# Optimization experiments

Hardware: AMD Instinct MI355X
Metric: run time of the kernel (lower is better)

## Reference

```python
import jax, jax.numpy as jnp
import numpy as np

B, S, H = 2, 2048, 1024
NQ, NKV, HD = 16, 4, 64
I, E, TOP_K = 3584, 8, 2
SLIDING_WINDOW = 512
EPS = 1e-5
MAX_WAVELENGTH = 10000.0


def setup_inputs() -> dict:
    key = jax.random.key(0)
    ks = jax.random.split(key, 10)
    p = lambda k, shape: jax.random.normal(k, shape, jnp.float32) * 0.02
    return {
        "decoder_sequence": jax.random.normal(ks[0], (B, S, H), jnp.float32),
        "norm1_scale": jnp.ones((H,), jnp.float32),
        "norm2_scale": jnp.ones((H,), jnp.float32),
        "wq": p(ks[1], (H, NQ, HD)),
        "wk": p(ks[2], (H, NKV, HD)),
        "wv": p(ks[3], (H, NKV, HD)),
        "wo": p(ks[4], (NQ, HD, H)),
        "w_router": p(ks[5], (H, E)),
        "w_gate": p(ks[6], (E, H, I)),
        "w_up": p(ks[7], (E, H, I)),
        "w_down": p(ks[8], (E, I, H)),
    }


def _rms_norm(x, scale, eps=EPS):
    x32 = x.astype(jnp.float32)
    var = jnp.mean(x32 * x32, axis=-1, keepdims=True)
    return (x32 * jax.lax.rsqrt(var + eps) * scale).astype(x.dtype)


def _rope(x):
    # x: [B, S, n_heads, head_dim]; keras-hub RotaryEmbedding (interleaved cos/sin,
    # half-split rotate then interleave via stack+reshape).
    seq_len, dim = x.shape[1], x.shape[3]
    inv_freq = 1.0 / (MAX_WAVELENGTH ** (jnp.arange(0, dim, 2, dtype=jnp.float32) / dim))
    freq = jnp.arange(seq_len, dtype=jnp.float32)[:, None] * inv_freq[None, :]  # [S, D/2]
    emb = jnp.stack((freq, freq), axis=-1).reshape(seq_len, dim)  # interleaved [S, D]
    cos = jnp.cos(emb)[None, :, None, :].astype(x.dtype)
    sin = jnp.sin(emb)[None, :, None, :].astype(x.dtype)
    x1, x2 = jnp.split(x, 2, axis=-1)
    half_rot = jnp.stack((-x2, x1), axis=-1).reshape(x.shape)
    return x * cos + half_rot * sin


def _forward(x, norm1_scale, norm2_scale, wq, wk, wv, wo, w_router, w_gate, w_up, w_down):
    b, s, h = x.shape
    # --- self attention block ---
    resid = x
    hs = _rms_norm(x, norm1_scale)
    q = jnp.einsum("bsh,hnd->bsnd", hs, wq)
    k = jnp.einsum("bsh,hnd->bsnd", hs, wk)
    v = jnp.einsum("bsh,hnd->bsnd", hs, wv)
    q, k = _rope(q), _rope(k)
    rep = q.shape[2] // k.shape[2]  # GQA group size
    k = jnp.repeat(k, rep, axis=2)
    v = jnp.repeat(v, rep, axis=2)
    scores = jnp.einsum("bqnd,bknd->bnqk", q, k) / jnp.sqrt(jnp.asarray(q.shape[-1], q.dtype))
    qi = jnp.arange(s)[:, None]
    ki = jnp.arange(s)[None, :]
    mask = (ki <= qi) & (ki > qi - SLIDING_WINDOW)  # causal + sliding window
    scores = jnp.where(mask[None, None], scores, jnp.asarray(-1e9, scores.dtype))
    probs = jax.nn.softmax(scores, axis=-1)
    attn = jnp.einsum("bnqk,bknd->bqnd", probs, v)
    x = jnp.einsum("bqnd,ndh->bqh", attn, wo) + resid
    # --- sparse MoE block ---
    resid = x
    hs = _rms_norm(x, norm2_scale)
    h2 = hs.reshape(-1, h)  # [T, H]
    router_logits = h2 @ w_router  # [T, E]
    rw = jax.nn.softmax(router_logits, axis=-1)
    topw, topi = jax.lax.top_k(rw, TOP_K)
    topw = topw / jnp.sum(topw, axis=-1, keepdims=True)
    t = h2.shape[0]
    combine = jnp.zeros((t, E), h2.dtype).at[jnp.arange(t)[:, None], topi].set(topw)
    out = jnp.zeros_like(h2)
    for e in range(E):  # fixed small expert loop; zero combine weight == not routed
        g = jax.nn.silu(h2 @ w_gate[e])
        u = h2 @ w_up[e]
        out = out + combine[:, e:e + 1] * ((u * g) @ w_down[e])
    decoder_output = out.reshape(b, s, h) + resid
    return decoder_output, router_logits


def reference(decoder_sequence, norm1_scale, norm2_scale, wq, wk, wv, wo,
              w_router, w_gate, w_up, w_down):
    return _forward(decoder_sequence, norm1_scale, norm2_scale, wq, wk, wv, wo,
                    w_router, w_gate, w_up, w_down)
```

## Files before the change

kernel.cpp:

```cpp
#include <hip/hip_runtime.h>
#include <hip/hip_bf16.h>
#include <cstdio>


typedef __bf16 bf16x8 __attribute__((ext_vector_type(8)));
typedef float f32x4 __attribute__((ext_vector_type(4)));

#define MFMA16(a, b, c) __builtin_amdgcn_mfma_f32_16x16x32_bf16((a), (b), (c), 0, 0, 0)
#define GL16(g, l)                                                             \
  __builtin_amdgcn_global_load_lds(                                            \
      (const __attribute__((address_space(1))) void*)(g),                      \
      (__attribute__((address_space(3))) void*)(l), 16, 0, 0)
#define WAIT_VM0() asm volatile("s_waitcnt vmcnt(0)" ::: "memory")
#define SETPRIO(n) __builtin_amdgcn_s_setprio(n)
#define PIPE_SYNC(n)                                                           \
  do {                                                                         \
    asm volatile("s_waitcnt vmcnt(" #n ")" ::: "memory");                      \
    __builtin_amdgcn_s_barrier();                                              \
    asm volatile("" ::: "memory");                                             \
  } while (0)

__device__ __forceinline__ unsigned short f2bf(float f) {
  unsigned u = __builtin_bit_cast(unsigned, f);
  u += 0x7fffu + ((u >> 16) & 1u);
  return (unsigned short)(u >> 16);
}
__device__ __forceinline__ float bf2f(unsigned short h) {
  unsigned u = ((unsigned)h) << 16;
  return __builtin_bit_cast(float, u);
}
__device__ __forceinline__ int sw32(int row, int chunk) {
  return row * 32 + ((chunk ^ ((row >> 1) & 3)) * 8);
}

static constexpr size_t O_WQKVT_HI = 0;
static constexpr size_t SZ_WQKVT   = 1536UL * 1024 * 2;
static constexpr size_t O_WQKVT_LO = O_WQKVT_HI + SZ_WQKVT;
static constexpr size_t O_WOT_HI   = O_WQKVT_LO + SZ_WQKVT;
static constexpr size_t SZ_WOT     = 1024UL * 1024 * 2;
static constexpr size_t O_WOT_LO   = O_WOT_HI + SZ_WOT;
static constexpr size_t O_WGT      = O_WOT_LO + SZ_WOT;
static constexpr size_t SZ_WE      = 8UL * 3584 * 1024 * 2;
static constexpr size_t O_WUT      = O_WGT + SZ_WE;
static constexpr size_t O_WDT      = O_WUT + SZ_WE;
static constexpr size_t O_H2       = O_WDT + SZ_WE;
static constexpr size_t SZ_BF_TH   = 4096UL * 1024 * 2;
static constexpr size_t O_TOK      = O_H2 + SZ_BF_TH;
static constexpr size_t O_WGTL     = O_TOK + 8UL * 4096 * 4;
static constexpr size_t O_CNT      = O_WGTL + 8UL * 4096 * 4;
static constexpr size_t O_DYN      = O_CNT + 256;
static constexpr size_t O_HSHI  = O_DYN;
static constexpr size_t O_HSLO  = O_HSHI + SZ_BF_TH;
static constexpr size_t O_QKV   = O_HSLO + SZ_BF_TH;
static constexpr size_t O_QHI   = O_QKV + 4096UL * 1536 * 4;
static constexpr size_t O_QLO   = O_QHI + SZ_BF_TH;
static constexpr size_t O_KHI   = O_QLO + SZ_BF_TH;
static constexpr size_t SZ_BF_T256 = 4096UL * 256 * 2;
static constexpr size_t O_KLO   = O_KHI + SZ_BF_T256;
static constexpr size_t O_VTH   = O_KLO + SZ_BF_T256;
static constexpr size_t O_VTL   = O_VTH + SZ_BF_T256;
static constexpr size_t O_AHI   = O_VTL + SZ_BF_T256;
static constexpr size_t O_ALO   = O_AHI + SZ_BF_TH;
static constexpr size_t O_XATTN = O_ALO + SZ_BF_TH;
static constexpr size_t O_END   = O_XATTN + 4096UL * 1024 * 4;
static constexpr size_t O_ACT   = O_DYN;
static constexpr size_t WS_NEED = O_END;

__global__ void zero_cnt_kernel(int* c) {
  if (threadIdx.x < 8) c[threadIdx.x] = 0;
}

__global__ __launch_bounds__(256) void init_out_kernel(const float* __restrict__ x,
                                                       float* __restrict__ o) {
  const long i = (long)blockIdx.x * 256 + threadIdx.x;
  *(float4*)&o[i * 4] = *(const float4*)&x[i * 4];
}

__global__ __launch_bounds__(256) void rmsnorm_kernel(const float* __restrict__ x,
                                                      const float* __restrict__ scale,
                                                      unsigned short* __restrict__ hi,
                                                      unsigned short* __restrict__ lo) {
  const int t = blockIdx.x, tid = threadIdx.x;
  const float4 v = *(const float4*)&x[(long)t * 1024 + tid * 4];
  float ss = v.x * v.x + v.y * v.y + v.z * v.z + v.w * v.w;
#pragma unroll
  for (int off = 32; off >= 1; off >>= 1) ss += __shfl_down(ss, off);
  __shared__ float red[4];
  if ((tid & 63) == 0) red[tid >> 6] = ss;
  __syncthreads();
  const float r = rsqrtf((red[0] + red[1] + red[2] + red[3]) * (1.0f / 1024.0f) + 1e-5f);
  const float4 sc = *(const float4*)&scale[tid * 4];
  float o[4] = {v.x * r * sc.x, v.y * r * sc.y, v.z * r * sc.z, v.w * r * sc.w};
  ushort4 hh, ll;
  unsigned short* hp = (unsigned short*)&hh;
  unsigned short* lp = (unsigned short*)&ll;
#pragma unroll
  for (int i = 0; i < 4; ++i) {
    hp[i] = f2bf(o[i]);
    lp[i] = f2bf(o[i] - bf2f(hp[i]));
  }
  *(ushort4*)&hi[(long)t * 1024 + tid * 4] = hh;
  if (lo) *(ushort4*)&lo[(long)t * 1024 + tid * 4] = ll;
}

__global__ __launch_bounds__(256) void transpose_cvt(const float* __restrict__ src,
                                                     unsigned short* __restrict__ dst,
                                                     int R, int C, long zsrc, long zdst) {
  src += (long)blockIdx.z * zsrc;
  dst += (long)blockIdx.z * zdst;
  const int c0 = blockIdx.x * 64, r0 = blockIdx.y * 64, tid = threadIdx.x;
  __shared__ float tb[64][65];
#pragma unroll
  for (int p = 0; p < 4; ++p) {
    const int r = p * 16 + (tid >> 4), c = (tid & 15) * 4;
    const float4 v = *(const float4*)&src[(long)(r0 + r) * C + c0 + c];
    tb[c + 0][r] = v.x; tb[c + 1][r] = v.y; tb[c + 2][r] = v.z; tb[c + 3][r] = v.w;
  }
  __syncthreads();
  const int dr = tid >> 2, s0 = (tid & 3) * 16;
  __align__(16) unsigned short tmp[16];
#pragma unroll
  for (int i = 0; i < 16; ++i) tmp[i] = f2bf(tb[dr][s0 + i]);
  const long o = (long)(c0 + dr) * R + r0 + s0;
  *(uint4*)&dst[o] = *(const uint4*)&tmp[0];
  *(uint4*)&dst[o + 8] = *(const uint4*)&tmp[8];
}

__global__ __launch_bounds__(256) void transpose_cvt_split(const float* __restrict__ src,
                                                           unsigned short* __restrict__ dh,
                                                           unsigned short* __restrict__ dl,
                                                           int R, int C) {
  const int c0 = blockIdx.x * 64, r0 = blockIdx.y * 64, tid = threadIdx.x;
  __shared__ float tb[64][65];
#pragma unroll
  for (int p = 0; p < 4; ++p) {
    const int r = p * 16 + (tid >> 4), c = (tid & 15) * 4;
    const float4 v = *(const float4*)&src[(long)(r0 + r) * C + c0 + c];
    tb[c + 0][r] = v.x; tb[c + 1][r] = v.y; tb[c + 2][r] = v.z; tb[c + 3][r] = v.w;
  }
  __syncthreads();
  const int dr = tid >> 2, s0 = (tid & 3) * 16;
  __align__(16) unsigned short th[16], tl[16];
#pragma unroll
  for (int i = 0; i < 16; ++i) {
    const float f = tb[dr][s0 + i];
    th[i] = f2bf(f);
    tl[i] = f2bf(f - bf2f(th[i]));
  }
  const long o = (long)(c0 + dr) * R + r0 + s0;
  *(uint4*)&dh[o] = *(const uint4*)&th[0];
  *(uint4*)&dh[o + 8] = *(const uint4*)&th[8];
  *(uint4*)&dl[o] = *(const uint4*)&tl[0];
  *(uint4*)&dl[o + 8] = *(const uint4*)&tl[8];
}

__global__ __launch_bounds__(256) void gemm_split(const unsigned short* __restrict__ Ahi,
                                                  const unsigned short* __restrict__ Alo,
                                                  const unsigned short* __restrict__ Bhi,
                                                  const unsigned short* __restrict__ Blo,
                                                  const float* __restrict__ resid,
                                                  float* __restrict__ C,
                                                  int M, int N, int K) {
  __shared__ unsigned short Ash[2][4096], Asl[2][4096], Bsh[2][4096], Bsl[2][4096];
  const int tid = threadIdx.x, wid = tid >> 6, lane = tid & 63;
  const int m0 = blockIdx.y * 128, n0 = blockIdx.x * 128;
  const int wm = (wid >> 1) * 64, wn = (wid & 1) * 64;
  const int fr = lane & 15, fg = lane >> 4;
  const int srow = tid >> 2;
  const int scol = (((tid & 3) ^ ((tid >> 3) & 3))) * 8;
  const long aoff = (long)(m0 + srow) * K + scol;
  const long boff = (long)(n0 + srow) * K + scol;
  const long h64 = 64L * K;
  char* a0 = (char*)Ash[0] + wid * 1024; char* a1 = (char*)Ash[1] + wid * 1024;
  char* al0 = (char*)Asl[0] + wid * 1024; char* al1 = (char*)Asl[1] + wid * 1024;
  char* b0 = (char*)Bsh[0] + wid * 1024; char* b1 = (char*)Bsh[1] + wid * 1024;
  char* bl0 = (char*)Bsl[0] + wid * 1024; char* bl1 = (char*)Bsl[1] + wid * 1024;
#define GS_STAGE(koff, pah_, pal_, pbh_, pbl_)                                 \
  do {                                                                         \
    GL16(Ahi + aoff + (koff), (pah_));                                         \
    GL16(Ahi + aoff + h64 + (koff), (pah_) + 4096);                            \
    GL16(Alo + aoff + (koff), (pal_));                                         \
    GL16(Alo + aoff + h64 + (koff), (pal_) + 4096);                            \
    GL16(Bhi + boff + (koff), (pbh_));                                         \
    GL16(Bhi + boff + h64 + (koff), (pbh_) + 4096);                            \
    GL16(Blo + boff + (koff), (pbl_));                                         \
    GL16(Blo + boff + h64 + (koff), (pbl_) + 4096);                            \
  } while (0)
  f32x4 acc[4][4] = {};
  GS_STAGE(0, a0, al0, b0, bl0);
  WAIT_VM0();
  __syncthreads();
  int cur = 0;
  for (int k0 = 0; k0 < K; k0 += 32) {
    const int kn = k0 + 32;
    if (kn < K) {
      if (cur) GS_STAGE(kn, a0, al0, b0, bl0);
      else     GS_STAGE(kn, a1, al1, b1, bl1);
    }
    const unsigned short* As_ = Ash[cur];
    const unsigned short* Al_ = Asl[cur];
    const unsigned short* Bs_ = Bsh[cur];
    const unsigned short* Bl_ = Bsl[cur];
    bf16x8 ah[4], al[4], bh[4], bl[4];
#pragma unroll
    for (int i = 0; i < 4; ++i) {
      const int oA = sw32(wm + i * 16 + fr, fg);
      const int oB = sw32(wn + i * 16 + fr, fg);
      ah[i] = *(const bf16x8*)&As_[oA];
      al[i] = *(const bf16x8*)&Al_[oA];
      bh[i] = *(const bf16x8*)&Bs_[oB];
      bl[i] = *(const bf16x8*)&Bl_[oB];
    }
    SETPRIO(1);
#pragma unroll
    for (int i = 0; i < 4; ++i)
#pragma unroll
      for (int j = 0; j < 4; ++j) {
        acc[i][j] = MFMA16(al[i], bh[j], acc[i][j]);
        acc[i][j] = MFMA16(ah[i], bl[j], acc[i][j]);
        acc[i][j] = MFMA16(ah[i], bh[j], acc[i][j]);
      }
    SETPRIO(0);
    WAIT_VM0();
    __syncthreads();
    cur ^= 1;
  }
#undef GS_STAGE
  const int cr = fg * 4;
#pragma unroll
  for (int i = 0; i < 4; ++i)
#pragma unroll
    for (int j = 0; j < 4; ++j)
#pragma unroll
      for (int rr = 0; rr < 4; ++rr) {
        const int row = m0 + wm + i * 16 + cr + rr;
        const int col = n0 + wn + j * 16 + fr;
        float v = acc[i][j][rr];
        if (resid) v += resid[(long)row * N + col];
        C[(long)row * N + col] = v;
      }
}

__global__ __launch_bounds__(256) void rope_kernel(const float* __restrict__ qkv,
                                                   unsigned short* __restrict__ Qh,
                                                   unsigned short* __restrict__ Ql,
                                                   unsigned short* __restrict__ Kh,
                                                   unsigned short* __restrict__ Kl) {
  const int t = blockIdx.x, b = t >> 11, s = t & 2047;
  const float* src = qkv + (long)t * 1536;
  for (int task = threadIdx.x; task < 640; task += 256) {
    const int head = task >> 5, p = task & 31;
    const float* hp = src + head * 64;
    const float inv = (float)exp2(-(double)p * 0.4152410118609203);
    const float f = (float)s * inv;
    float sn, cs;
    sincosf(f, &sn, &cs);
    const float x0 = hp[2 * p], x1 = hp[2 * p + 1], xa = hp[p], xb = hp[32 + p];
    float o0 = x0 * cs - xb * sn;
    float o1 = x1 * cs + xa * sn;
    unsigned short *dh, *dl;
    long base;
    if (head < 16) {
      o0 *= 0.125f; o1 *= 0.125f;
      base = ((long)(b * 16 + head) * 2048 + s) * 64;
      dh = Qh; dl = Ql;
    } else {
      base = ((long)(b * 4 + (head - 16)) * 2048 + s) * 64;
      dh = Kh; dl = Kl;
    }
    unsigned short h0 = f2bf(o0);
    dh[base + 2 * p] = h0; dl[base + 2 * p] = f2bf(o0 - bf2f(h0));
    unsigned short h1 = f2bf(o1);
    dh[base + 2 * p + 1] = h1; dl[base + 2 * p + 1] = f2bf(o1 - bf2f(h1));
  }
}

__global__ __launch_bounds__(256) void vt_split_kernel(const float* __restrict__ qkv,
                                                       unsigned short* __restrict__ Vh,
                                                       unsigned short* __restrict__ Vl) {
  const int st = blockIdx.x * 64, g = blockIdx.y, b = blockIdx.z, tid = threadIdx.x;
  __shared__ float tb[64][65];
  const float* src = qkv + (long)(b * 2048 + st) * 1536 + 1280 + g * 64;
#pragma unroll
  for (int p = 0; p < 4; ++p) {
    const int r = p * 16 + (tid >> 4), c = (tid & 15) * 4;
    const float4 v = *(const float4*)&src[(long)r * 1536 + c];
    tb[c + 0][r] = v.x; tb[c + 1][r] = v.y; tb[c + 2][r] = v.z; tb[c + 3][r] = v.w;
  }
  __syncthreads();
  const int dr = tid >> 2, s0 = (tid & 3) * 16;
  __align__(16) unsigned short hh[16], ll[16];
#pragma unroll
  for (int i = 0; i < 16; ++i) {
    const float f = tb[dr][s0 + i];
    hh[i] = f2bf(f);
    ll[i] = f2bf(f - bf2f(hh[i]));
  }
  const long dst = ((long)(b * 4 + g) * 64 + dr) * 2048 + st + s0;
  *(uint4*)&Vh[dst] = *(const uint4*)&hh[0];
  *(uint4*)&Vh[dst + 8] = *(const uint4*)&hh[8];
  *(uint4*)&Vl[dst] = *(const uint4*)&ll[0];
  *(uint4*)&Vl[dst + 8] = *(const uint4*)&ll[8];
}

__global__ __launch_bounds__(256) void attn_kernel(const unsigned short* __restrict__ Qh,
                                                   const unsigned short* __restrict__ Ql,
                                                   const unsigned short* __restrict__ Kh,
                                                   const unsigned short* __restrict__ Kl,
                                                   const unsigned short* __restrict__ Vh,
                                                   const unsigned short* __restrict__ Vl,
                                                   unsigned short* __restrict__ Ohi,
                                                   unsigned short* __restrict__ Olo) {
  const int qt = blockIdx.x, h = blockIdx.y, b = blockIdx.z, g = h >> 2;
  const int q0 = qt * 64, tid = threadIdx.x, wid = tid >> 6, lane = tid & 63;
  const int fr = lane & 15, fg = lane >> 4;
  __shared__ unsigned short Ksh[2][2048], Ksl[2][2048];
  __shared__ unsigned short Vsh[2][2048], Vsl[2][2048];
  __shared__ unsigned short Ph[4][512], Pl[4][512];

  const long qoff = ((long)(b * 16 + h) * 2048 + q0 + wid * 16 + fr) * 64;
  bf16x8 qh[2], ql[2];
  qh[0] = *(const bf16x8*)&Qh[qoff + fg * 8];
  qh[1] = *(const bf16x8*)&Qh[qoff + 32 + fg * 8];
  ql[0] = *(const bf16x8*)&Ql[qoff + fg * 8];
  ql[1] = *(const bf16x8*)&Ql[qoff + 32 + fg * 8];

  f32x4 o[4] = {};
  float mrow[4], lrow[4];
#pragma unroll
  for (int rr = 0; rr < 4; ++rr) { mrow[rr] = -1e30f; lrow[rr] = 0.f; }

  const int jmin = (q0 >= 511) ? (q0 - 511) : 0;
  const int jt0 = jmin & ~31;
  const long kbase = ((long)(b * 4 + g) * 2048) * 64;
  const long vbase = ((long)(b * 4 + g) * 64) * 2048;
  const int srK = tid >> 3;
  const int scK = (((tid & 7) ^ (srK & 7))) * 8;
  const int srV = tid >> 2;
  const int scV = (((tid & 3) ^ ((srV >> 1) & 3))) * 8;
  char* kh0 = (char*)Ksh[0] + wid * 1024; char* kh1 = (char*)Ksh[1] + wid * 1024;
  char* kl0 = (char*)Ksl[0] + wid * 1024; char* kl1 = (char*)Ksl[1] + wid * 1024;
  char* vh0 = (char*)Vsh[0] + wid * 1024; char* vh1 = (char*)Vsh[1] + wid * 1024;
  char* vl0 = (char*)Vsl[0] + wid * 1024; char* vl1 = (char*)Vsl[1] + wid * 1024;
#define ATTN_STAGE(jt_, kh_, kl_, vh_, vl_)                                    \
  do {                                                                         \
    const long ko = kbase + (long)((jt_) + srK) * 64 + scK;                    \
    GL16(Kh + ko, (kh_));                                                      \
    GL16(Kl + ko, (kl_));                                                      \
    const long vo = vbase + (long)srV * 2048 + (jt_) + scV;                    \
    GL16(Vh + vo, (vh_));                                                      \
    GL16(Vl + vo, (vl_));                                                      \
  } while (0)

  ATTN_STAGE(jt0, kh0, kl0, vh0, vl0);
  WAIT_VM0();
  __syncthreads();
  int cur = 0;
  for (int jt = jt0; jt < q0 + 64; jt += 32) {
    const int jn = jt + 32;
    if (jn < q0 + 64) {
      if (cur) ATTN_STAGE(jn, kh0, kl0, vh0, vl0);
      else     ATTN_STAGE(jn, kh1, kl1, vh1, vl1);
    }
    const unsigned short* KH = Ksh[cur];
    const unsigned short* KL = Ksl[cur];
    const unsigned short* VH = Vsh[cur];
    const unsigned short* VL = Vsl[cur];

    f32x4 sf[2] = {};
#pragma unroll
    for (int cf = 0; cf < 2; ++cf)
#pragma unroll
      for (int dc = 0; dc < 2; ++dc) {
        const int row = cf * 16 + fr;
        const int off = row * 64 + (((dc * 4 + fg) ^ (row & 7)) * 8);
        const bf16x8 kh = *(const bf16x8*)&KH[off];
        const bf16x8 kl = *(const bf16x8*)&KL[off];
        sf[cf] = MFMA16(ql[dc], kh, sf[cf]);
        sf[cf] = MFMA16(qh[dc], kl, sf[cf]);
        sf[cf] = MFMA16(qh[dc], kh, sf[cf]);
      }

    float sv[2][4];
#pragma unroll
    for (int cf = 0; cf < 2; ++cf) {
      const int j = jt + cf * 16 + fr;
#pragma unroll
      for (int rr = 0; rr < 4; ++rr) {
        const int q = q0 + wid * 16 + fg * 4 + rr;
        const bool ok = (j <= q) && (j >= q - 511);
        sv[cf][rr] = ok ? sf[cf][rr] : -1e30f;
      }
    }
    float scl_[4];
#pragma unroll
    for (int rr = 0; rr < 4; ++rr) {
      float mx = fmaxf(sv[0][rr], sv[1][rr]);
      mx = fmaxf(mx, __shfl_xor(mx, 1));
      mx = fmaxf(mx, __shfl_xor(mx, 2));
      mx = fmaxf(mx, __shfl_xor(mx, 4));
      mx = fmaxf(mx, __shfl_xor(mx, 8));
      const float mn = fmaxf(mrow[rr], mx);
      scl_[rr] = __expf(mrow[rr] - mn);
      mrow[rr] = mn;
    }
    float ps[2][4], rs[4] = {0.f, 0.f, 0.f, 0.f};
#pragma unroll
    for (int cf = 0; cf < 2; ++cf)
#pragma unroll
      for (int rr = 0; rr < 4; ++rr) {
        const float p = (sv[cf][rr] > -1e29f) ? __expf(sv[cf][rr] - mrow[rr]) : 0.f;
        ps[cf][rr] = p;
        rs[rr] += p;
      }
#pragma unroll
    for (int rr = 0; rr < 4; ++rr) {
      float r = rs[rr];
      r += __shfl_xor(r, 1);
      r += __shfl_xor(r, 2);
      r += __shfl_xor(r, 4);
      r += __shfl_xor(r, 8);
      lrow[rr] = lrow[rr] * scl_[rr] + r;
      o[0][rr] *= scl_[rr]; o[1][rr] *= scl_[rr];
      o[2][rr] *= scl_[rr]; o[3][rr] *= scl_[rr];
    }
#pragma unroll
    for (int cf = 0; cf < 2; ++cf)
#pragma unroll
      for (int rr = 0; rr < 4; ++rr) {
        const int q = fg * 4 + rr, k = cf * 16 + fr;
        const int idx = q * 32 + (((k >> 3) ^ ((q >> 1) & 3)) * 8) + (k & 7);
        const unsigned short hb = f2bf(ps[cf][rr]);
        Ph[wid][idx] = hb;
        Pl[wid][idx] = f2bf(ps[cf][rr] - bf2f(hb));
      }
    const int pro = sw32(fr, fg);
    const bf16x8 pah = *(const bf16x8*)&Ph[wid][pro];
    const bf16x8 pal = *(const bf16x8*)&Pl[wid][pro];
#pragma unroll
    for (int df = 0; df < 4; ++df) {
      const int vo = sw32(df * 16 + fr, fg);
      const bf16x8 vh = *(const bf16x8*)&VH[vo];
      const bf16x8 vl = *(const bf16x8*)&VL[vo];
      o[df] = MFMA16(pal, vh, o[df]);
      o[df] = MFMA16(pah, vl, o[df]);
      o[df] = MFMA16(pah, vh, o[df]);
    }
    WAIT_VM0();
    __syncthreads();
    cur ^= 1;
  }
#undef ATTN_STAGE
#pragma unroll
  for (int df = 0; df < 4; ++df)
#pragma unroll
    for (int rr = 0; rr < 4; ++rr) {
      const int q = q0 + wid * 16 + fg * 4 + rr;
      const float v = o[df][rr] / lrow[rr];
      const long oi = ((long)(b * 2048 + q)) * 1024 + h * 64 + df * 16 + fr;
      const unsigned short hb = f2bf(v);
      Ohi[oi] = hb;
      Olo[oi] = f2bf(v - bf2f(hb));
    }
}

__global__ __launch_bounds__(256) void router_kernel(const float* __restrict__ xattn,
                                                     const float* __restrict__ scale,
                                                     const float* __restrict__ wr,
                                                     float* __restrict__ logits,
                                                     int* __restrict__ tok,
                                                     float* __restrict__ wgt,
                                                     int* __restrict__ cnt) {
  const int t = blockIdx.x, tid = threadIdx.x;
  const float4 v = *(const float4*)&xattn[(long)t * 1024 + tid * 4];
  float ss = v.x * v.x + v.y * v.y + v.z * v.z + v.w * v.w;
#pragma unroll
  for (int off = 32; off >= 1; off >>= 1) ss += __shfl_down(ss, off);
  __shared__ float red[4];
  __shared__ float redE[4][8];
  __shared__ float lg[8];
  if ((tid & 63) == 0) red[tid >> 6] = ss;
  __syncthreads();
  const float r = rsqrtf((red[0] + red[1] + red[2] + red[3]) * (1.0f / 1024.0f) + 1e-5f);
  const float4 sc = *(const float4*)&scale[tid * 4];
  const float hv[4] = {v.x * r * sc.x, v.y * r * sc.y, v.z * r * sc.z, v.w * r * sc.w};
  float part[8];
#pragma unroll
  for (int e = 0; e < 8; ++e) part[e] = 0.f;
#pragma unroll
  for (int i = 0; i < 4; ++i) {
    const float* w = &wr[(long)(tid * 4 + i) * 8];
#pragma unroll
    for (int e = 0; e < 8; ++e) part[e] = fmaf(hv[i], w[e], part[e]);
  }
#pragma unroll
  for (int off = 32; off >= 1; off >>= 1)
#pragma unroll
    for (int e = 0; e < 8; ++e) part[e] += __shfl_down(part[e], off);
  if ((tid & 63) == 0)
#pragma unroll
    for (int e = 0; e < 8; ++e) redE[tid >> 6][e] = part[e];
  __syncthreads();
  if (tid < 8) {
    const float l8 = redE[0][tid] + redE[1][tid] + redE[2][tid] + redE[3][tid];
    lg[tid] = l8;
    logits[(long)t * 8 + tid] = l8;
  }
  __syncthreads();
  if (tid == 0) {
    float mx = lg[0];
#pragma unroll
    for (int e = 1; e < 8; ++e) mx = fmaxf(mx, lg[e]);
    float p[8];
#pragma unroll
    for (int e = 0; e < 8; ++e) p[e] = __expf(lg[e] - mx);
    int i1 = 0;
#pragma unroll
    for (int e = 1; e < 8; ++e) if (p[e] > p[i1]) i1 = e;
    int i2 = (i1 == 0) ? 1 : 0;
#pragma unroll
    for (int e = 0; e < 8; ++e) if (e != i2 && e != i1 && p[e] > p[i2]) i2 = e;
    const float wsum = p[i1] + p[i2];
    const float w1 = p[i1] / wsum, w2 = p[i2] / wsum;
    const int pos1 = atomicAdd(&cnt[i1], 1);
    tok[i1 * 4096 + pos1] = t; wgt[i1 * 4096 + pos1] = w1;
    const int pos2 = atomicAdd(&cnt[i2], 1);
    tok[i2 * 4096 + pos2] = t; wgt[i2 * 4096 + pos2] = w2;
  }
}

__global__ __launch_bounds__(512, 2) void gateup_kernel(const unsigned short* __restrict__ H2,
                                                        const unsigned short* __restrict__ WG,
                                                        const unsigned short* __restrict__ WU,
                                                        const int* __restrict__ tok,
                                                        const int* __restrict__ cnt,
                                                        unsigned short* __restrict__ act) {
  const int e = blockIdx.z;
  const int cn = cnt[e];
  const int m0 = blockIdx.y * 256;
  if (m0 >= cn) return;
  int padoff = 0;
  for (int i = 0; i < e; ++i) padoff += (cnt[i] + 255) & ~255;
  const int n0 = blockIdx.x * 128;
  __shared__ unsigned short As[3][8192], Bg[3][4096], Bu[3][4096];
  const int tid = threadIdx.x, wid = tid >> 6, lane = tid & 63;
  const int wm = (wid >> 2) * 128, wn = (wid & 3) * 32;
  const int fr = lane & 15, fg = lane >> 4;
  const int srow = tid >> 2;
  const int scol = (((tid & 3) ^ ((tid >> 3) & 3))) * 8;
  const int lr1 = m0 + srow, lr2 = lr1 + 128;
  const int tok1 = (lr1 < cn) ? tok[e * 4096 + lr1] : 0;
  const int tok2 = (lr2 < cn) ? tok[e * 4096 + lr2] : 0;
  const unsigned short* ga1 = H2 + (long)tok1 * 1024 + scol;
  const unsigned short* ga2 = H2 + (long)tok2 * 1024 + scol;
  const unsigned short* gb = WG + (long)e * 3584 * 1024 + (long)(n0 + srow) * 1024 + scol;
  const unsigned short* gu = WU + (long)e * 3584 * 1024 + (long)(n0 + srow) * 1024 + scol;
#define GU_STAGE(s, b)                                                         \
  do {                                                                         \
    const int ko = (s) * 32;                                                   \
    GL16(ga1 + ko, (char*)As[b] + wid * 1024);                                 \
    GL16(ga2 + ko, (char*)As[b] + 8192 + wid * 1024);                          \
    GL16(gb + ko, (char*)Bg[b] + wid * 1024);                                  \
    GL16(gu + ko, (char*)Bu[b] + wid * 1024);                                  \
  } while (0)
  f32x4 ag[8][2] = {}, au[8][2] = {};
  GU_STAGE(0, 0);
  GU_STAGE(1, 1);
  PIPE_SYNC(4);
  for (int t = 0; t < 32; ++t) {
    const int cb = t % 3;
    if (t + 2 < 32) GU_STAGE(t + 2, (t + 2) % 3);
    const unsigned short* As_ = As[cb];
    const unsigned short* Bg_ = Bg[cb];
    const unsigned short* Bu_ = Bu[cb];
    bf16x8 af[8], bgf[2], buf_[2];
#pragma unroll
    for (int i = 0; i < 8; ++i) af[i] = *(const bf16x8*)&As_[sw32(wm + i * 16 + fr, fg)];
#pragma unroll
    for (int j = 0; j < 2; ++j) {
      const int oB = sw32(wn + j * 16 + fr, fg);
      bgf[j] = *(const bf16x8*)&Bg_[oB];
      buf_[j] = *(const bf16x8*)&Bu_[oB];
    }
    SETPRIO(1);
#pragma unroll
    for (int i = 0; i < 8; ++i)
#pragma unroll
      for (int j = 0; j < 2; ++j) {
        ag[i][j] = MFMA16(af[i], bgf[j], ag[i][j]);
        au[i][j] = MFMA16(af[i], buf_[j], au[i][j]);
      }
    SETPRIO(0);
    if (t + 2 < 32) PIPE_SYNC(4);
    else if (t + 1 < 32) PIPE_SYNC(0);
  }
#undef GU_STAGE
  const int cr = fg * 4;
#pragma unroll
  for (int i = 0; i < 8; ++i)
#pragma unroll
    for (int j = 0; j < 2; ++j)
#pragma unroll
      for (int rr = 0; rr < 4; ++rr) {
        const int row = wm + i * 16 + cr + rr;
        const int col = n0 + wn + j * 16 + fr;
        const float gv = ag[i][j][rr];
        const float sg = gv / (1.f + __expf(-gv));
        act[(long)(padoff + m0 + row) * 3584 + col] = f2bf(sg * au[i][j][rr]);
      }
}

__global__ __launch_bounds__(512, 4) void down_kernel(const unsigned short* __restrict__ act,
                                                      const unsigned short* __restrict__ WD,
                                                      const int* __restrict__ tok,
                                                      const float* __restrict__ wgt,
                                                      const int* __restrict__ cnt,
                                                      float* __restrict__ out) {
  const int e = blockIdx.z;
  const int cn = cnt[e];
  const int m0 = blockIdx.y * 128;
  if (m0 >= cn) return;
  int padoff = 0;
  for (int i = 0; i < e; ++i) padoff += (cnt[i] + 255) & ~255;
  const int n0 = blockIdx.x * 256;
  __shared__ unsigned short As[3][4096], Bs[3][8192];
  const int tid = threadIdx.x, wid = tid >> 6, lane = tid & 63;
  const int wm = (wid >> 2) * 64, wn = (wid & 3) * 64;
  const int fr = lane & 15, fg = lane >> 4;
  const int srow = tid >> 2;
  const int scol = (((tid & 3) ^ ((tid >> 3) & 3))) * 8;
  const unsigned short* ga = act + (long)(padoff + m0 + srow) * 3584 + scol;
  const unsigned short* gb = WD + (long)e * 1024 * 3584 + (long)(n0 + srow) * 3584 + scol;
#define DN_STAGE(s, b)                                                         \
  do {                                                                         \
    const int ko = (s) * 32;                                                   \
    GL16(ga + ko, (char*)As[b] + wid * 1024);                                  \
    GL16(gb + ko, (char*)Bs[b] + wid * 1024);                                  \
    GL16(gb + 128L * 3584 + ko, (char*)Bs[b] + 8192 + wid * 1024);             \
  } while (0)
  f32x4 acc[4][4] = {};
  DN_STAGE(0, 0);
  DN_STAGE(1, 1);
  PIPE_SYNC(3);
  for (int t = 0; t < 112; ++t) {
    const int cb = t % 3;
    if (t + 2 < 112) DN_STAGE(t + 2, (t + 2) % 3);
    const unsigned short* As_ = As[cb];
    const unsigned short* Bs_ = Bs[cb];
    bf16x8 af[4], bf_[4];
#pragma unroll
    for (int i = 0; i < 4; ++i) af[i] = *(const bf16x8*)&As_[sw32(wm + i * 16 + fr, fg)];
#pragma unroll
    for (int j = 0; j < 4; ++j) bf_[j] = *(const bf16x8*)&Bs_[sw32(wn + j * 16 + fr, fg)];
    SETPRIO(1);
#pragma unroll
    for (int i = 0; i < 4; ++i)
#pragma unroll
      for (int j = 0; j < 4; ++j)
        acc[i][j] = MFMA16(af[i], bf_[j], acc[i][j]);
    SETPRIO(0);
    if (t + 2 < 112) PIPE_SYNC(3);
    else if (t + 1 < 112) PIPE_SYNC(0);
  }
#undef DN_STAGE
  const int cr = fg * 4;
#pragma unroll
  for (int i = 0; i < 4; ++i)
#pragma unroll
    for (int rr = 0; rr < 4; ++rr) {
      const int lrow = m0 + wm + i * 16 + cr + rr;
      if (lrow < cn) {
        const int tk = tok[e * 4096 + lrow];
        const float w = wgt[e * 4096 + lrow];
#pragma unroll
        for (int j = 0; j < 4; ++j)
          atomicAdd(&out[(long)tk * 1024 + n0 + wn + j * 16 + fr], w * acc[i][j][rr]);
      }
    }
}

extern "C" void kernel_launch(void* const* d_in, const int* in_sizes, int n_in,
                              void* d_out, int out_size, void* d_ws, size_t ws_size,
                              hipStream_t stream) {
  (void)in_sizes; (void)n_in; (void)out_size;
  if (ws_size < WS_NEED) {
    fprintf(stderr, "kernel_launch: ws too small: %zu < %zu\n", ws_size, (size_t)WS_NEED);
  }
  const float* x    = (const float*)d_in[0];
  const float* n1s  = (const float*)d_in[1];
  const float* n2s  = (const float*)d_in[2];
  const float* wq   = (const float*)d_in[3];
  const float* wk   = (const float*)d_in[4];
  const float* wv   = (const float*)d_in[5];
  const float* wo   = (const float*)d_in[6];
  const float* wrt  = (const float*)d_in[7];
  const float* wg   = (const float*)d_in[8];
  const float* wu   = (const float*)d_in[9];
  const float* wd   = (const float*)d_in[10];
  float* out = (float*)d_out;
  char* W = (char*)d_ws;

  unsigned short* WQH = (unsigned short*)(W + O_WQKVT_HI);
  unsigned short* WQL = (unsigned short*)(W + O_WQKVT_LO);
  unsigned short* WOH = (unsigned short*)(W + O_WOT_HI);
  unsigned short* WOL = (unsigned short*)(W + O_WOT_LO);
  unsigned short* WGT = (unsigned short*)(W + O_WGT);
  unsigned short* WUT = (unsigned short*)(W + O_WUT);
  unsigned short* WDT = (unsigned short*)(W + O_WDT);
  unsigned short* H2  = (unsigned short*)(W + O_H2);
  int* TOK    = (int*)(W + O_TOK);
  float* WGTL = (float*)(W + O_WGTL);
  int* CNT    = (int*)(W + O_CNT);
  unsigned short* HSH = (unsigned short*)(W + O_HSHI);
  unsigned short* HSL = (unsigned short*)(W + O_HSLO);
  float* QKV = (float*)(W + O_QKV);
  unsigned short* QHI = (unsigned short*)(W + O_QHI);
  unsigned short* QLO = (unsigned short*)(W + O_QLO);
  unsigned short* KHI = (unsigned short*)(W + O_KHI);
  unsigned short* KLO = (unsigned short*)(W + O_KLO);
  unsigned short* VTH = (unsigned short*)(W + O_VTH);
  unsigned short* VTL = (unsigned short*)(W + O_VTL);
  unsigned short* AHI = (unsigned short*)(W + O_AHI);
  unsigned short* ALO = (unsigned short*)(W + O_ALO);
  float* XATTN = (float*)(W + O_XATTN);
  unsigned short* ACT = (unsigned short*)(W + O_ACT);

  zero_cnt_kernel<<<1, 64, 0, stream>>>(CNT);
  rmsnorm_kernel<<<4096, 256, 0, stream>>>(x, n1s, HSH, HSL);
  transpose_cvt_split<<<dim3(16, 16, 1), 256, 0, stream>>>(wq, WQH, WQL, 1024, 1024);
  transpose_cvt_split<<<dim3(4, 16, 1), 256, 0, stream>>>(wk, WQH + 1024L * 1024, WQL + 1024L * 1024, 1024, 256);
  transpose_cvt_split<<<dim3(4, 16, 1), 256, 0, stream>>>(wv, WQH + 1280L * 1024, WQL + 1280L * 1024, 1024, 256);
  transpose_cvt_split<<<dim3(16, 16, 1), 256, 0, stream>>>(wo, WOH, WOL, 1024, 1024);
  transpose_cvt<<<dim3(56, 16, 8), 256, 0, stream>>>(wg, WGT, 1024, 3584, 1024L * 3584, 3584L * 1024);
  transpose_cvt<<<dim3(56, 16, 8), 256, 0, stream>>>(wu, WUT, 1024, 3584, 1024L * 3584, 3584L * 1024);
  transpose_cvt<<<dim3(16, 56, 8), 256, 0, stream>>>(wd, WDT, 3584, 1024, 3584L * 1024, 1024L * 3584);
  gemm_split<<<dim3(12, 32, 1), 256, 0, stream>>>(HSH, HSL, WQH, WQL, nullptr, QKV, 4096, 1536, 1024);
  rope_kernel<<<4096, 256, 0, stream>>>(QKV, QHI, QLO, KHI, KLO);
  vt_split_kernel<<<dim3(32, 4, 2), 256, 0, stream>>>(QKV, VTH, VTL);
  attn_kernel<<<dim3(32, 16, 2), 256, 0, stream>>>(QHI, QLO, KHI, KLO, VTH, VTL, AHI, ALO);
  gemm_split<<<dim3(8, 32, 1), 256, 0, stream>>>(AHI, ALO, WOH, WOL, x, XATTN, 4096, 1024, 1024);
  rmsnorm_kernel<<<4096, 256, 0, stream>>>(XATTN, n2s, H2, nullptr);
  router_kernel<<<4096, 256, 0, stream>>>(XATTN, n2s, wrt, out + 4194304, TOK, WGTL, CNT);
  init_out_kernel<<<4096, 256, 0, stream>>>(XATTN, out);
  gateup_kernel<<<dim3(28, 16, 8), 512, 0, stream>>>(H2, WGT, WUT, TOK, CNT, ACT);
  down_kernel<<<dim3(4, 32, 8), 512, 0, stream>>>(ACT, WDT, TOK, WGTL, CNT, out);
}
```

Baseline: 782.0 us.

## Restructure MoE gate/up GEMM into ping-pong 4-phase pipeline with split gate/up warps

Rewrites the gate/up expert GEMM to use BK=64 double-buffered LDS with an 8-chunk XOR swizzle. Each warp group now computes either the gate or the up matrix over a 128x64 sub-tile instead of both. Each k-step is split into four interleaved phases of global prefetch, LDS fragment loads and MFMA clusters, separated by barriers, so memory traffic overlaps compute. The SiLU combine goes through an LDS exchange where gate warps write fp32 results and up warps read them. This adds more barriers per iteration and a 128 KB LDS footprint, which may limit occupancy to one block per CU despite the launch bound of 2.

```diff
diff --git a/kernel.cpp b/kernel.cpp
--- a/kernel.cpp
+++ b/kernel.cpp
@@ -13,6 +13,17 @@
       (__attribute__((address_space(3))) void*)(l), 16, 0, 0)
 #define WAIT_VM0() asm volatile("s_waitcnt vmcnt(0)" ::: "memory")
 #define SETPRIO(n) __builtin_amdgcn_s_setprio(n)
+#define BAR()                                                                  \
+  do {                                                                         \
+    asm volatile("" ::: "memory");                                             \
+    __builtin_amdgcn_s_barrier();                                              \
+    asm volatile("" ::: "memory");                                             \
+  } while (0)
+#define LGKM0()                                                                \
+  do {                                                                         \
+    asm volatile("s_waitcnt lgkmcnt(0)" ::: "memory");                         \
+    __builtin_amdgcn_sched_barrier(0);                                         \
+  } while (0)
 #define PIPE_SYNC(n)                                                           \
   do {                                                                         \
     asm volatile("s_waitcnt vmcnt(" #n ")" ::: "memory");                      \
@@ -542,72 +553,152 @@
   int padoff = 0;
   for (int i = 0; i < e; ++i) padoff += (cnt[i] + 255) & ~255;
   const int n0 = blockIdx.x * 128;
-  __shared__ unsigned short As[3][8192], Bg[3][4096], Bu[3][4096];
+  __shared__ char LB[131072];
+  char* A0 = LB;            char* A1 = LB + 32768;
+  char* B0 = LB + 65536;    char* B1 = LB + 98304;
   const int tid = threadIdx.x, wid = tid >> 6, lane = tid & 63;
-  const int wm = (wid >> 2) * 128, wn = (wid & 3) * 32;
+  const int mat = wid >> 2;
+  const int wm = ((wid >> 1) & 1) * 128;
+  const int wn = (wid & 1) * 64;
   const int fr = lane & 15, fg = lane >> 4;
-  const int srow = tid >> 2;
-  const int scol = (((tid & 3) ^ ((tid >> 3) & 3))) * 8;
-  const int lr1 = m0 + srow, lr2 = lr1 + 128;
-  const int tok1 = (lr1 < cn) ? tok[e * 4096 + lr1] : 0;
-  const int tok2 = (lr2 < cn) ? tok[e * 4096 + lr2] : 0;
-  const unsigned short* ga1 = H2 + (long)tok1 * 1024 + scol;
-  const unsigned short* ga2 = H2 + (long)tok2 * 1024 + scol;
-  const unsigned short* gb = WG + (long)e * 3584 * 1024 + (long)(n0 + srow) * 1024 + scol;
-  const unsigned short* gu = WU + (long)e * 3584 * 1024 + (long)(n0 + srow) * 1024 + scol;
-#define GU_STAGE(s, b)                                                         \
-  do {                                                                         \
-    const int ko = (s) * 32;                                                   \
-    GL16(ga1 + ko, (char*)As[b] + wid * 1024);                                 \
-    GL16(ga2 + ko, (char*)As[b] + 8192 + wid * 1024);                          \
-    GL16(gb + ko, (char*)Bg[b] + wid * 1024);                                  \
-    GL16(gu + ko, (char*)Bu[b] + wid * 1024);                                  \
-  } while (0)
-  f32x4 ag[8][2] = {}, au[8][2] = {};
-  GU_STAGE(0, 0);
-  GU_STAGE(1, 1);
-  PIPE_SYNC(4);
-  for (int t = 0; t < 32; ++t) {
-    const int cb = t % 3;
-    if (t + 2 < 32) GU_STAGE(t + 2, (t + 2) % 3);
-    const unsigned short* As_ = As[cb];
-    const unsigned short* Bg_ = Bg[cb];
-    const unsigned short* Bu_ = Bu[cb];
-    bf16x8 af[8], bgf[2], buf_[2];
-#pragma unroll
-    for (int i = 0; i < 8; ++i) af[i] = *(const bf16x8*)&As_[sw32(wm + i * 16 + fr, fg)];
+  const int sc = ((tid & 7) ^ ((tid >> 3) & 7)) * 8;
+  const unsigned short* gap0; const unsigned short* gap1;
+  const unsigned short* gap2; const unsigned short* gap3;
+  {
+    const int r0_ = m0 + 0 * 64 + (tid >> 3), r1_ = m0 + 1 * 64 + (tid >> 3);
+    const int r2_ = m0 + 2 * 64 + (tid >> 3), r3_ = m0 + 3 * 64 + (tid >> 3);
+    gap0 = H2 + (long)((r0_ < cn) ? tok[e * 4096 + r0_] : 0) * 1024 + sc;
+    gap1 = H2 + (long)((r1_ < cn) ? tok[e * 4096 + r1_] : 0) * 1024 + sc;
+    gap2 = H2 + (long)((r2_ < cn) ? tok[e * 4096 + r2_] : 0) * 1024 + sc;
+    gap3 = H2 + (long)((r3_ < cn) ? tok[e * 4096 + r3_] : 0) * 1024 + sc;
+  }
+  const long eoffW = (long)e * 3584 * 1024;
+  const unsigned short* gbp0 = WG + eoffW + (long)(n0 + 0 + (tid >> 3)) * 1024 + sc;
+  const unsigned short* gbp1 = WG + eoffW + (long)(n0 + 64 + (tid >> 3)) * 1024 + sc;
+  const unsigned short* gbp2 = WU + eoffW + (long)(n0 + 0 + (tid >> 3)) * 1024 + sc;
+  const unsigned short* gbp3 = WU + eoffW + (long)(n0 + 64 + (tid >> 3)) * 1024 + sc;
+#define GU_A(pg, dst, c, ko) GL16((pg) + (ko), (dst) + (c) * 8192 + wid * 1024)
+  const int csw0 = (0 * 64 + fg * 16) ^ ((fr & 7) << 4);
+  const int csw1 = (1 * 64 + fg * 16) ^ ((fr & 7) << 4);
+
+  f32x4 acc[8][4] = {};
+  GU_A(gap0, A0, 0, 0); GU_A(gap1, A0, 1, 0); GU_A(gap2, A0, 2, 0); GU_A(gap3, A0, 3, 0);
+  GU_A(gbp0, B0, 0, 0); GU_A(gbp1, B0, 1, 0); GU_A(gbp2, B0, 2, 0); GU_A(gbp3, B0, 3, 0);
+  WAIT_VM0();
+  BAR();
+
+  for (int t = 0; t < 16; ++t) {
+    const char* Ac = (t & 1) ? A1 : A0;
+    const char* Bc = (t & 1) ? B1 : B0;
+    char* An = (t & 1) ? A0 : A1;
+    char* Bn = (t & 1) ? B0 : B1;
+    const int ko = (t + 1) * 64;
+    const bool pre = (t < 15);
+    bf16x8 af[8], bf0[4], bf1[4];
+    if (pre) { GU_A(gap0, An, 0, ko); GU_A(gap1, An, 1, ko); GU_A(gbp0, Bn, 0, ko); }
+#pragma unroll
+    for (int i = 0; i < 4; ++i) {
+      const int lr = wm + i * 16 + fr;
+      af[i * 2 + 0] = *(const bf16x8*)&Ac[lr * 128 + csw0];
+      af[i * 2 + 1] = *(const bf16x8*)&Ac[lr * 128 + csw1];
+    }
 #pragma unroll
     for (int j = 0; j < 2; ++j) {
-      const int oB = sw32(wn + j * 16 + fr, fg);
-      bgf[j] = *(const bf16x8*)&Bg_[oB];
-      buf_[j] = *(const bf16x8*)&Bu_[oB];
-    }
+      const int lr = mat * 128 + wn + j * 16 + fr;
+      bf0[j * 2 + 0] = *(const bf16x8*)&Bc[lr * 128 + csw0];
+      bf0[j * 2 + 1] = *(const bf16x8*)&Bc[lr * 128 + csw1];
+    }
+    BAR();
+    LGKM0();
     SETPRIO(1);
 #pragma unroll
-    for (int i = 0; i < 8; ++i)
+    for (int i = 0; i < 4; ++i)
 #pragma unroll
       for (int j = 0; j < 2; ++j) {
-        ag[i][j] = MFMA16(af[i], bgf[j], ag[i][j]);
-        au[i][j] = MFMA16(af[i], buf_[j], au[i][j]);
+        acc[i][j] = MFMA16(af[i * 2 + 0], bf0[j * 2 + 0], acc[i][j]);
+        acc[i][j] = MFMA16(af[i * 2 + 1], bf0[j * 2 + 1], acc[i][j]);
       }
     SETPRIO(0);
-    if (t + 2 < 32) PIPE_SYNC(4);
-    else if (t + 1 < 32) PIPE_SYNC(0);
-  }
-#undef GU_STAGE
-  const int cr = fg * 4;
-#pragma unroll
-  for (int i = 0; i < 8; ++i)
-#pragma unroll
-    for (int j = 0; j < 2; ++j)
-#pragma unroll
-      for (int rr = 0; rr < 4; ++rr) {
-        const int row = wm + i * 16 + cr + rr;
-        const int col = n0 + wn + j * 16 + fr;
-        const float gv = ag[i][j][rr];
-        const float sg = gv / (1.f + __expf(-gv));
-        act[(long)(padoff + m0 + row) * 3584 + col] = f2bf(sg * au[i][j][rr]);
-      }
+    BAR();
+    if (pre) { GU_A(gap2, An, 2, ko); GU_A(gap3, An, 3, ko); GU_A(gbp1, Bn, 1, ko); }
+#pragma unroll
+    for (int j = 0; j < 2; ++j) {
+      const int lr = mat * 128 + wn + 32 + j * 16 + fr;
+      bf1[j * 2 + 0] = *(const bf16x8*)&Bc[lr * 128 + csw0];
+      bf1[j * 2 + 1] = *(const bf16x8*)&Bc[lr * 128 + csw1];
+    }
+    BAR();
+    LGKM0();
+    SETPRIO(1);
+#pragma unroll
+    for (int i = 0; i < 4; ++i)
+#pragma unroll
+      for (int j = 0; j < 2; ++j) {
+        acc[i][2 + j] = MFMA16(af[i * 2 + 0], bf1[j * 2 + 0], acc[i][2 + j]);
+        acc[i][2 + j] = MFMA16(af[i * 2 + 1], bf1[j * 2 + 1], acc[i][2 + j]);
+      }
+    SETPRIO(0);
+    BAR();
+    if (pre) { GU_A(gbp2, Bn, 2, ko); GU_A(gbp3, Bn, 3, ko); }
+#pragma unroll
+    for (int i = 0; i < 4; ++i) {
+      const int lr = wm + 64 + i * 16 + fr;
+      af[i * 2 + 0] = *(const bf16x8*)&Ac[lr * 128 + csw0];
+      af[i * 2 + 1] = *(const bf16x8*)&Ac[lr * 128 + csw1];
+    }
+    BAR();
+    LGKM0();
+    SETPRIO(1);
+#pragma unroll
+    for (int i = 0; i < 4; ++i)
+#pragma unroll
+      for (int j = 0; j < 2; ++j) {
+        acc[4 + i][2 + j] = MFMA16(af[i * 2 + 0], bf1[j * 2 + 0], acc[4 + i][2 + j]);
+        acc[4 + i][2 + j] = MFMA16(af[i * 2 + 1], bf1[j * 2 + 1], acc[4 + i][2 + j]);
+      }
+    SETPRIO(0);
+    BAR();
+    SETPRIO(1);
+#pragma unroll
+    for (int i = 0; i < 4; ++i)
+#pragma unroll
+      for (int j = 0; j < 2; ++j) {
+        acc[4 + i][j] = MFMA16(af[i * 2 + 0], bf0[j * 2 + 0], acc[4 + i][j]);
+        acc[4 + i][j] = MFMA16(af[i * 2 + 1], bf0[j * 2 + 1], acc[4 + i][j]);
+      }
+    SETPRIO(0);
+    if (pre) WAIT_VM0();
+    BAR();
+  }
+#undef GU_A
+  float* G = (float*)LB;
+  if (mat == 0) {
+#pragma unroll
+    for (int mf = 0; mf < 8; ++mf)
+#pragma unroll
+      for (int nf = 0; nf < 4; ++nf)
+#pragma unroll
+        for (int rr = 0; rr < 4; ++rr) {
+          const int row = wm + (mf >> 2) * 64 + (mf & 3) * 16 + fg * 4 + rr;
+          const int col = wn + nf * 16 + fr;
+          G[row * 128 + col] = acc[mf][nf][rr];
+        }
+  }
+  BAR();
+  if (mat == 1) {
+#pragma unroll
+    for (int mf = 0; mf < 8; ++mf)
+#pragma unroll
+      for (int nf = 0; nf < 4; ++nf)
+#pragma unroll
+        for (int rr = 0; rr < 4; ++rr) {
+          const int row = wm + (mf >> 2) * 64 + (mf & 3) * 16 + fg * 4 + rr;
+          const int col = wn + nf * 16 + fr;
+          const float gv = G[row * 128 + col];
+          const float sg = gv / (1.f + __expf(-gv));
+          act[(long)(padoff + m0 + row) * 3584 + n0 + col] = f2bf(sg * acc[mf][nf][rr]);
+        }
+  }
 }
 
 __global__ __launch_bounds__(512, 4) void down_kernel(const unsigned short* __restrict__ act,
```

Result: faster. 753.2 us (-3.7%).
